# Kernel optimization log

Measured on AMD Instinct MI355X. Metric: run time of the kernel, lower is better.

Reference implementation:

```python
import jax, jax.numpy as jnp
import numpy as np

N = 50000      # nodes
F = 128        # in_features
OUT = 128      # out_features
E = 600000     # edges per adjacency (avg degree 12)
J = 2
BN_EPS = 1e-5


def setup_inputs() -> dict:
    key = jax.random.key(0)
    ks = jax.random.split(key, 10)
    x = jax.random.normal(ks[0], (N, F), dtype=jnp.float32)
    rows0 = jax.random.randint(ks[1], (E,), 0, N, dtype=jnp.int32)
    cols0 = jax.random.randint(ks[2], (E,), 0, N, dtype=jnp.int32)
    vals0 = jax.random.uniform(ks[3], (E,), dtype=jnp.float32)
    rows1 = jax.random.randint(ks[4], (E,), 0, N, dtype=jnp.int32)
    cols1 = jax.random.randint(ks[5], (E,), 0, N, dtype=jnp.int32)
    vals1 = jax.random.uniform(ks[6], (E,), dtype=jnp.float32)
    # Linear(J*F, OUT) params, torch default init U(-1/sqrt(fan_in), 1/sqrt(fan_in))
    lim = 1.0 / np.sqrt(J * F)
    W_fc = jax.random.uniform(ks[7], (OUT, J * F), dtype=jnp.float32, minval=-lim, maxval=lim)
    b_fc = jax.random.uniform(ks[8], (OUT,), dtype=jnp.float32, minval=-lim, maxval=lim)
    gamma = jnp.ones((OUT,), dtype=jnp.float32)
    beta = jnp.zeros((OUT,), dtype=jnp.float32)
    return {"x": x, "rows0": rows0, "cols0": cols0, "vals0": vals0,
            "rows1": rows1, "cols1": cols1, "vals1": vals1,
            "W_fc": W_fc, "b_fc": b_fc, "gamma": gamma, "beta": beta}


def _spmm(rows, cols, vals, x):
    # sparse [N,N] @ dense [N,F]: gather source features, weight, scatter-add to rows
    msgs = vals[:, None] * x[cols]                      # [E, F]
    return jax.ops.segment_sum(msgs, rows, num_segments=x.shape[0])  # [N, F]


def reference(x, rows0, cols0, vals0, rows1, cols1, vals1, W_fc, b_fc, gamma, beta):
    h = jnp.concatenate([_spmm(rows0, cols0, vals0, x),
                         _spmm(rows1, cols1, vals1, x)], axis=1)  # [N, J*F]
    y = h @ W_fc.T + b_fc                                         # [N, OUT]
    # BatchNorm1d (training mode: batch stats, biased variance)
    mean = jnp.mean(y, axis=0)
    var = jnp.mean((y - mean) ** 2, axis=0)
    return (y - mean) * jax.lax.rsqrt(var + BN_EPS) * gamma + beta
```

## Files before the change

### kernel.cpp

```cpp
#include <hip/hip_runtime.h>

#define N_NODES 50000
#define F_IN 128
#define OUT_F 128
#define JF 256
#define EDGES 600000
#define BN_EPS 1e-5f
#define MAXDEG 48
#define NPART 8
#define PART_ROWS 6250
#define CHUNK_E 2048
#define NCHUNK 586

#define SCAT_B (NPART * NCHUNK)
#define CONVX_B 6250
#define CONVW_B 32
#define BUILD_B (SCAT_B + CONVX_B + CONVW_B)
#define ROWS_PB 32
#define GATH_B 1563
#define GROWS 64
#define GEMM_B 782
#define HPAD 50048
#define NCOPY 16

typedef __attribute__((ext_vector_type(8))) short short8;
typedef __attribute__((ext_vector_type(4))) float floatx4;
typedef __attribute__((ext_vector_type(4))) unsigned short ushortx4;

static __device__ __forceinline__ unsigned short f2bf(float f) {
    unsigned int x = __float_as_uint(f);
    unsigned int r = (x + 0x7fffu + ((x >> 16) & 1u)) >> 16;
    return (unsigned short)r;
}
static __device__ __forceinline__ float bflo(unsigned int p) { return __uint_as_float(p << 16); }
static __device__ __forceinline__ float bfhi(unsigned int p) { return __uint_as_float(p & 0xffff0000u); }

__global__ __launch_bounds__(256) void build_kernel(
    const int* __restrict__ rows0, const int* __restrict__ cols0, const float* __restrict__ vals0,
    const int* __restrict__ rows1, const int* __restrict__ cols1, const float* __restrict__ vals1,
    int* __restrict__ cnt0, int* __restrict__ cnt1,
    unsigned int* __restrict__ pe0, unsigned int* __restrict__ pe1,
    const floatx4* __restrict__ x4, ushortx4* __restrict__ xb4,
    const float* __restrict__ W, uint2* __restrict__ Wb2)
{
    int bid = blockIdx.x;
    int tid = threadIdx.x;
    if (bid < SCAT_B) {
        unsigned part = (unsigned)(bid & (NPART - 1));
        int c0 = (bid >> 3) * CHUNK_E;

        bool pure0 = (c0 + CHUNK_E <= EDGES);
        bool pure1 = (c0 >= EDGES) && (c0 + CHUNK_E <= 2 * EDGES);
        if (pure0 || pure1) {
            const int*   rows = pure1 ? rows1 : rows0;
            const int*   cols = pure1 ? cols1 : cols0;
            const float* vals = pure1 ? vals1 : vals0;
            int*          cnt = pure1 ? cnt1 : cnt0;
            unsigned int*  pe = pure1 ? pe1 : pe0;
            int eb = pure1 ? c0 - EDGES : c0;
            #pragma unroll
            for (int g = 0; g < 2; ++g) {
                int e = eb + g * 1024 + tid * 4;
                int4 rv = *(const int4*)(rows + e);
                int rr[4] = {rv.x, rv.y, rv.z, rv.w};
                #pragma unroll
                for (int j = 0; j < 4; ++j) {
                    int r = rr[j];
                    if ((unsigned)r / (unsigned)PART_ROWS == part) {
                        int ee = e + j;
                        int c = cols[ee];
                        float v = vals[ee];
                        int p = atomicAdd(&cnt[r], 1);
                        if (p < MAXDEG)
                            pe[(size_t)r * MAXDEG + p] = ((unsigned int)c << 16) | f2bf(v);
                    }
                }
            }
        } else {
            for (int i = 0; i < CHUNK_E / 256; ++i) {
                int e = c0 + i * 256 + tid;
                if (e < 2 * EDGES) {
                    bool s1 = e >= EDGES;
                    int ee = s1 ? e - EDGES : e;
                    int r = s1 ? rows1[ee] : rows0[ee];
                    if ((unsigned)r / (unsigned)PART_ROWS == part) {
                        int c = s1 ? cols1[ee] : cols0[ee];
                        float v = s1 ? vals1[ee] : vals0[ee];
                        int* cnt = s1 ? cnt1 : cnt0;
                        unsigned int* pe = s1 ? pe1 : pe0;
                        int p = atomicAdd(&cnt[r], 1);
                        if (p < MAXDEG)
                            pe[(size_t)r * MAXDEG + p] = ((unsigned int)c << 16) | f2bf(v);
                    }
                }
            }
        }
    } else if (bid < SCAT_B + CONVX_B) {
        int i = (bid - SCAT_B) * 256 + tid;
        floatx4 v = __builtin_nontemporal_load(&x4[i]);
        ushortx4 o;
        o.x = f2bf(v.x); o.y = f2bf(v.y); o.z = f2bf(v.z); o.w = f2bf(v.w);
        __builtin_nontemporal_store(o, &xb4[i]);
    } else {
        int i = (bid - SCAT_B - CONVX_B) * 256 + tid;
        int col = i >> 6, l = i & 63;
        const float* wr = W + (size_t)col * JF;
        float a0 = wr[2 * l], a1 = wr[2 * l + 1];
        float b0 = wr[128 + 2 * l], b1 = wr[128 + 2 * l + 1];
        uint2 o;
        o.x = (unsigned int)f2bf(a0) | ((unsigned int)f2bf(a1) << 16);
        o.y = (unsigned int)f2bf(b0) | ((unsigned int)f2bf(b1) << 16);
        Wb2[col * 64 + l] = o;
    }
}

static __device__ __forceinline__ void rec_u(
    unsigned int q, int lane,
    const unsigned int* __restrict__ xb32, float& A0, float& A1)
{
    unsigned int xv = xb32[(q >> 16) * 64 + lane];
    float vv = __uint_as_float(q << 16);
    A0 += vv * bflo(xv);
    A1 += vv * bfhi(xv);
}
static __device__ __forceinline__ void rec_m(
    unsigned int q, bool on, int lane,
    const unsigned int* __restrict__ xb32, float& A0, float& A1)
{
    unsigned int idx = on ? (q >> 16) : 0u;
    float vv = on ? __uint_as_float(q << 16) : 0.0f;
    unsigned int xv = xb32[idx * 64 + lane];
    A0 += vv * bflo(xv);
    A1 += vv * bfhi(xv);
}

__global__ __launch_bounds__(256, 8) void gather_kernel(
    const unsigned int* __restrict__ xb32,
    const int* __restrict__ cnt0, const unsigned int* __restrict__ pe0,
    const int* __restrict__ cnt1, const unsigned int* __restrict__ pe1,
    uint2* __restrict__ hb)
{
    __shared__ uint4 recs[2][ROWS_PB][6];
    __shared__ int   lcnt[2][ROWS_PB];

    int tid = threadIdx.x;
    int lane = tid & 63;
    int w = tid >> 6;
    int wu = __builtin_amdgcn_readfirstlane(w);
    int row0 = blockIdx.x * ROWS_PB;

    {
        int idx = tid;
        #pragma unroll
        for (int pass = 0; pass < 2; ++pass) {
            if (idx < 384) {
                int lr = idx / 12;
                int rem = idx - lr * 12;
                int side = rem >= 6;
                int g = rem - side * 6;
                int r = row0 + lr; if (r >= N_NODES) r = N_NODES - 1;
                const unsigned int* pe = side ? pe1 : pe0;
                recs[side][lr][g] = *(const uint4*)(pe + (size_t)r * MAXDEG + g * 4);
            }
            idx += 256;
        }
        if (tid < 64) {
            int side = tid >= ROWS_PB;
            int lr = tid & (ROWS_PB - 1);
            int r = row0 + lr;
            int d = 0;
            if (r < N_NODES) d = (side ? cnt1 : cnt0)[r];
            if (d > MAXDEG) d = MAXDEG;
            lcnt[side][lr] = d;
        }
    }
    __syncthreads();

    for (int rr = 0; rr < 8; ++rr) {
        int lr = wu * 8 + rr;
        int r = row0 + lr;
        int d0 = __builtin_amdgcn_readfirstlane(lcnt[0][lr]);
        int d1 = __builtin_amdgcn_readfirstlane(lcnt[1][lr]);

        float aL0 = 0.f, aL1 = 0.f, aR0 = 0.f, aR1 = 0.f;

        #pragma unroll
        for (int g = 0; g < 6; ++g) {
            if (g * 4 < d0) {
                uint4 q = recs[0][lr][g];
                rec_u(q.x, lane, xb32, aL0, aL1);
                rec_m(q.y, g * 4 + 1 < d0, lane, xb32, aL0, aL1);
                rec_m(q.z, g * 4 + 2 < d0, lane, xb32, aL0, aL1);
                rec_m(q.w, g * 4 + 3 < d0, lane, xb32, aL0, aL1);
            }
        }
        #pragma unroll
        for (int g = 0; g < 6; ++g) {
            if (g * 4 < d1) {
                uint4 q = recs[1][lr][g];
                rec_u(q.x, lane, xb32, aR0, aR1);
                rec_m(q.y, g * 4 + 1 < d1, lane, xb32, aR0, aR1);
                rec_m(q.z, g * 4 + 2 < d1, lane, xb32, aR0, aR1);
                rec_m(q.w, g * 4 + 3 < d1, lane, xb32, aR0, aR1);
            }
        }
        if (d0 > 24)
            for (int p = 24; p < d0; ++p)
                rec_u(pe0[(size_t)r * MAXDEG + p], lane, xb32, aL0, aL1);
        if (d1 > 24)
            for (int p = 24; p < d1; ++p)
                rec_u(pe1[(size_t)r * MAXDEG + p], lane, xb32, aR0, aR1);

        uint2 o;
        o.x = (unsigned int)f2bf(aL0) | ((unsigned int)f2bf(aL1) << 16);
        o.y = (unsigned int)f2bf(aR0) | ((unsigned int)f2bf(aR1) << 16);
        hb[(size_t)(row0 + lr) * 64 + lane] = o;
    }
}

__global__ __launch_bounds__(256, 4) void gemm_kernel(
    const uint4* __restrict__ hb4,
    const ushort* __restrict__ Wb,
    const float* __restrict__ bias,
    float* __restrict__ y, float* __restrict__ stats)
{
    __shared__ char hsu[GROWS * 512];
    __shared__ float lstat[256];

    int tid = threadIdx.x;
    int lane = tid & 63;
    int w = tid >> 6;
    int row0 = blockIdx.x * GROWS;

    lstat[tid] = 0.f;

    const char* src = (const char*)hb4 + (size_t)row0 * 512;
    #pragma unroll
    for (int u = tid; u < GROWS * 32; u += 256) {
        int off = u * 16;
        int row = off >> 9;
        int dst = off ^ ((row & 7) << 4);
        *(uint4*)(hsu + dst) = *(const uint4*)(src + off);
    }
    __syncthreads();

    floatx4 acc[8];
    #pragma unroll
    for (int c = 0; c < 8; ++c) acc[c] = (floatx4){0.f, 0.f, 0.f, 0.f};

    int colb = lane & 15;
    int kg = lane >> 4;
    int arow = w * 16 + colb;
    unsigned int asw = (unsigned int)((arow & 7) << 4);

    #pragma unroll
    for (int k0 = 0; k0 < 8; ++k0) {
        short8 a = *(const short8*)(hsu + (((unsigned int)(arow * 512 + k0 * 64 + kg * 16)) ^ asw));
        #pragma unroll
        for (int c = 0; c < 8; ++c) {
            short8 b = *(const short8*)(Wb + (size_t)(c * 16 + colb) * 256 + k0 * 32 + kg * 8);
            acc[c] = __builtin_amdgcn_mfma_f32_16x16x32_bf16(a, b, acc[c], 0, 0, 0);
        }
    }

    int rq = kg * 4;
    #pragma unroll
    for (int c = 0; c < 8; ++c) {
        int col = c * 16 + colb;
        float bv = bias[col];
        float s = 0.f, s2 = 0.f;
        #pragma unroll
        for (int q = 0; q < 4; ++q) {
            int row = row0 + w * 16 + rq + q;
            if (row < N_NODES) {
                float val = acc[c][q] + bv;
                y[(size_t)row * OUT_F + col] = val;
                s += val; s2 += val * val;
            }
        }
        atomicAdd(&lstat[col], s);
        atomicAdd(&lstat[128 + col], s2);
    }
    __syncthreads();
    float* sdst = stats + (size_t)(blockIdx.x & (NCOPY - 1)) * 256;
    atomicAdd(&sdst[tid], lstat[tid]);
}

__global__ void bn_prep(const float* __restrict__ stats,
                        const float* __restrict__ gamma,
                        const float* __restrict__ beta,
                        float* __restrict__ ss)
{
    int o = threadIdx.x;
    if (o >= OUT_F) return;
    float s = 0.f, s2 = 0.f;
    #pragma unroll
    for (int c = 0; c < NCOPY; ++c) {
        s  += stats[c * 256 + o];
        s2 += stats[c * 256 + 128 + o];
    }
    float inv_n = 1.0f / (float)N_NODES;
    float mean = s * inv_n;
    float var  = s2 * inv_n - mean * mean;
    float sc = rsqrtf(var + BN_EPS) * gamma[o];
    ss[o] = sc;
    ss[OUT_F + o] = beta[o] - mean * sc;
}

__global__ __launch_bounds__(256) void bn_apply(
    float* __restrict__ y, const float* __restrict__ ss)
{
    size_t i = (size_t)blockIdx.x * blockDim.x + threadIdx.x;
    size_t total = (size_t)N_NODES * OUT_F / 4;
    if (i >= total) return;

    int c4 = (int)(i & (OUT_F / 4 - 1));
    float4 v  = ((const float4*)y)[i];
    float4 sc = ((const float4*)ss)[c4];
    float4 sh = ((const float4*)(ss + OUT_F))[c4];
    v.x = v.x * sc.x + sh.x;
    v.y = v.y * sc.y + sh.y;
    v.z = v.z * sc.z + sh.z;
    v.w = v.w * sc.w + sh.w;
    ((float4*)y)[i] = v;
}

extern "C" void kernel_launch(void* const* d_in, const int* in_sizes, int n_in,
                              void* d_out, int out_size, void* d_ws, size_t ws_size,
                              hipStream_t stream)
{
    const float* x     = (const float*)d_in[0];
    const int*   rows0 = (const int*)  d_in[1];
    const int*   cols0 = (const int*)  d_in[2];
    const float* vals0 = (const float*)d_in[3];
    const int*   rows1 = (const int*)  d_in[4];
    const int*   cols1 = (const int*)  d_in[5];
    const float* vals1 = (const float*)d_in[6];
    const float* W     = (const float*)d_in[7];
    const float* b     = (const float*)d_in[8];
    const float* gamma = (const float*)d_in[9];
    const float* beta  = (const float*)d_in[10];

    float* y = (float*)d_out;

    ushort* xb = (ushort*)d_ws;
    ushort* Wb = xb + (size_t)N_NODES * F_IN;
    unsigned int* pe0 = (unsigned int*)(Wb + OUT_F * JF);
    unsigned int* pe1 = pe0 + (size_t)N_NODES * MAXDEG;
    uint2* hb = (uint2*)(pe1 + (size_t)N_NODES * MAXDEG);
    int* cnt0 = (int*)(hb + (size_t)HPAD * 64);
    int* cnt1 = cnt0 + N_NODES;
    float* stats = (float*)(cnt1 + N_NODES);
    float* ss    = stats + NCOPY * 256;

    hipMemsetAsync(cnt0, 0, (2 * (size_t)N_NODES + NCOPY * 256) * sizeof(int), stream);

    build_kernel<<<BUILD_B, 256, 0, stream>>>(
        rows0, cols0, vals0, rows1, cols1, vals1,
        cnt0, cnt1, pe0, pe1,
        (const floatx4*)x, (ushortx4*)xb, W, (uint2*)Wb);

    gather_kernel<<<GATH_B, 256, 0, stream>>>(
        (const unsigned int*)xb, cnt0, pe0, cnt1, pe1, hb);

    gemm_kernel<<<GEMM_B, 256, 0, stream>>>(
        (const uint4*)hb, Wb, b, y, stats);

    bn_prep<<<1, 128, 0, stream>>>(stats, gamma, beta, ss);
    bn_apply<<<CONVX_B, 256, 0, stream>>>(y, ss);
}
```

Measured before the change: 182.1 us.

## Replace 8-pass partitioned edge scatter with two-phase bucket sort by row partition

```diff
diff --git a/kernel.cpp b/kernel.cpp
--- a/kernel.cpp
+++ b/kernel.cpp
@@ -9,15 +9,16 @@
 #define MAXDEG 48
 #define NPART 8
 #define PART_ROWS 6250
-#define CHUNK_E 2048
-#define NCHUNK 586
-
-#define SCAT_B (NPART * NCHUNK)
+#define BKCAP 163840
+#define LCAP 256
+#define EB_PER_SIDE 586
+#define EDGE_B (2*EB_PER_SIDE)
 #define CONVX_B 6250
 #define CONVW_B 32
-#define BUILD_B (SCAT_B + CONVX_B + CONVW_B)
-#define ROWS_PB 32
-#define GATH_B 1563
+#define BUILDA_B (EDGE_B + CONVX_B + CONVW_B)
+#define SCATB_B 1024
+#define ROWS_PB 16
+#define GATH_B 3125
 #define GROWS 64
 #define GEMM_B 782
 #define HPAD 50048
@@ -35,74 +36,75 @@
 static __device__ __forceinline__ float bflo(unsigned int p) { return __uint_as_float(p << 16); }
 static __device__ __forceinline__ float bfhi(unsigned int p) { return __uint_as_float(p & 0xffff0000u); }
 
-__global__ __launch_bounds__(256) void build_kernel(
+__global__ __launch_bounds__(256) void build_a(
     const int* __restrict__ rows0, const int* __restrict__ cols0, const float* __restrict__ vals0,
     const int* __restrict__ rows1, const int* __restrict__ cols1, const float* __restrict__ vals1,
-    int* __restrict__ cnt0, int* __restrict__ cnt1,
-    unsigned int* __restrict__ pe0, unsigned int* __restrict__ pe1,
+    uint2* __restrict__ buckets, int* __restrict__ gcur,
     const floatx4* __restrict__ x4, ushortx4* __restrict__ xb4,
     const float* __restrict__ W, uint2* __restrict__ Wb2)
 {
     int bid = blockIdx.x;
     int tid = threadIdx.x;
-    if (bid < SCAT_B) {
-        unsigned part = (unsigned)(bid & (NPART - 1));
-        int c0 = (bid >> 3) * CHUNK_E;
-
-        bool pure0 = (c0 + CHUNK_E <= EDGES);
-        bool pure1 = (c0 >= EDGES) && (c0 + CHUNK_E <= 2 * EDGES);
-        if (pure0 || pure1) {
-            const int*   rows = pure1 ? rows1 : rows0;
-            const int*   cols = pure1 ? cols1 : cols0;
-            const float* vals = pure1 ? vals1 : vals0;
-            int*          cnt = pure1 ? cnt1 : cnt0;
-            unsigned int*  pe = pure1 ? pe1 : pe0;
-            int eb = pure1 ? c0 - EDGES : c0;
+    if (bid < EDGE_B) {
+        __shared__ int   lcnt_[NPART];
+        __shared__ int   lbase[NPART];
+        __shared__ uint2 lbuf[NPART][LCAP];
+
+        if (tid < NPART) lcnt_[tid] = 0;
+        __syncthreads();
+
+        int side = bid >= EB_PER_SIDE;
+        int b = side ? bid - EB_PER_SIDE : bid;
+        const int*   rows = side ? rows1 : rows0;
+        const int*   cols = side ? cols1 : cols0;
+        const float* vals = side ? vals1 : vals0;
+
+        int e = b * 1024 + tid * 4;
+        if (e < EDGES) {
+            int4 rv = *(const int4*)(rows + e);
+            int4 cv = *(const int4*)(cols + e);
+            float4 vv = *(const float4*)(vals + e);
+            int rr[4] = {rv.x, rv.y, rv.z, rv.w};
+            int cc[4] = {cv.x, cv.y, cv.z, cv.w};
+            float ff[4] = {vv.x, vv.y, vv.z, vv.w};
             #pragma unroll
-            for (int g = 0; g < 2; ++g) {
-                int e = eb + g * 1024 + tid * 4;
-                int4 rv = *(const int4*)(rows + e);
-                int rr[4] = {rv.x, rv.y, rv.z, rv.w};
-                #pragma unroll
-                for (int j = 0; j < 4; ++j) {
-                    int r = rr[j];
-                    if ((unsigned)r / (unsigned)PART_ROWS == part) {
-                        int ee = e + j;
-                        int c = cols[ee];
-                        float v = vals[ee];
-                        int p = atomicAdd(&cnt[r], 1);
-                        if (p < MAXDEG)
-                            pe[(size_t)r * MAXDEG + p] = ((unsigned int)c << 16) | f2bf(v);
-                    }
+            for (int j = 0; j < 4; ++j) {
+                unsigned part = (unsigned)rr[j] / (unsigned)PART_ROWS;
+                uint2 q;
+                q.x = (unsigned)rr[j] | ((unsigned)side << 20);
+                q.y = ((unsigned)cc[j] << 16) | f2bf(ff[j]);
+                int pos = atomicAdd(&lcnt_[part], 1);
+                if (pos < LCAP) {
+                    lbuf[part][pos] = q;
+                } else {
+                    int gp = atomicAdd(&gcur[part], 1);
+                    if (gp < BKCAP) buckets[(size_t)part * BKCAP + gp] = q;
                 }
             }
-        } else {
-            for (int i = 0; i < CHUNK_E / 256; ++i) {
-                int e = c0 + i * 256 + tid;
-                if (e < 2 * EDGES) {
-                    bool s1 = e >= EDGES;
-                    int ee = s1 ? e - EDGES : e;
-                    int r = s1 ? rows1[ee] : rows0[ee];
-                    if ((unsigned)r / (unsigned)PART_ROWS == part) {
-                        int c = s1 ? cols1[ee] : cols0[ee];
-                        float v = s1 ? vals1[ee] : vals0[ee];
-                        int* cnt = s1 ? cnt1 : cnt0;
-                        unsigned int* pe = s1 ? pe1 : pe0;
-                        int p = atomicAdd(&cnt[r], 1);
-                        if (p < MAXDEG)
-                            pe[(size_t)r * MAXDEG + p] = ((unsigned int)c << 16) | f2bf(v);
-                    }
-                }
-            }
-        }
-    } else if (bid < SCAT_B + CONVX_B) {
-        int i = (bid - SCAT_B) * 256 + tid;
+        }
+        __syncthreads();
+        if (tid < NPART) {
+            int c = lcnt_[tid]; if (c > LCAP) c = LCAP;
+            lcnt_[tid] = c;
+            lbase[tid] = atomicAdd(&gcur[tid], c);
+        }
+        __syncthreads();
+        #pragma unroll
+        for (int p = 0; p < NPART; ++p) {
+            int c = lcnt_[p], base = lbase[p];
+            for (int j = tid; j < c; j += 256) {
+                int gp = base + j;
+                if (gp < BKCAP) buckets[(size_t)p * BKCAP + gp] = lbuf[p][j];
+            }
+        }
+    } else if (bid < EDGE_B + CONVX_B) {
+        int i = (bid - EDGE_B) * 256 + tid;
         floatx4 v = __builtin_nontemporal_load(&x4[i]);
         ushortx4 o;
         o.x = f2bf(v.x); o.y = f2bf(v.y); o.z = f2bf(v.z); o.w = f2bf(v.w);
         __builtin_nontemporal_store(o, &xb4[i]);
     } else {
-        int i = (bid - SCAT_B - CONVX_B) * 256 + tid;
+        int i = (bid - EDGE_B - CONVX_B) * 256 + tid;
         int col = i >> 6, l = i & 63;
         const float* wr = W + (size_t)col * JF;
         float a0 = wr[2 * l], a1 = wr[2 * l + 1];
@@ -114,6 +116,26 @@
     }
 }
 
+__global__ __launch_bounds__(256) void build_b(
+    const uint2* __restrict__ buckets, const int* __restrict__ gcur,
+    int* __restrict__ cnt0, int* __restrict__ cnt1,
+    unsigned int* __restrict__ pe0, unsigned int* __restrict__ pe1)
+{
+    int part = blockIdx.x & (NPART - 1);
+    int sub = blockIdx.x >> 3;
+    int n = gcur[part]; if (n > BKCAP) n = BKCAP;
+    const uint2* bk = buckets + (size_t)part * BKCAP;
+    for (int i = sub * 256 + threadIdx.x; i < n; i += (SCATB_B / NPART) * 256) {
+        uint2 q = bk[i];
+        unsigned r = q.x & 0xFFFFFu;
+        unsigned side = q.x >> 20;
+        int* cnt = side ? cnt1 : cnt0;
+        unsigned int* pe = side ? pe1 : pe0;
+        int p = atomicAdd(&cnt[r], 1);
+        if (p < MAXDEG) pe[(size_t)r * MAXDEG + p] = q.y;
+    }
+}
+
 static __device__ __forceinline__ void rec_u(
     unsigned int q, int lane,
     const unsigned int* __restrict__ xb32, float& A0, float& A1)
@@ -149,35 +171,25 @@
     int wu = __builtin_amdgcn_readfirstlane(w);
     int row0 = blockIdx.x * ROWS_PB;
 
-    {
-        int idx = tid;
-        #pragma unroll
-        for (int pass = 0; pass < 2; ++pass) {
-            if (idx < 384) {
-                int lr = idx / 12;
-                int rem = idx - lr * 12;
-                int side = rem >= 6;
-                int g = rem - side * 6;
-                int r = row0 + lr; if (r >= N_NODES) r = N_NODES - 1;
-                const unsigned int* pe = side ? pe1 : pe0;
-                recs[side][lr][g] = *(const uint4*)(pe + (size_t)r * MAXDEG + g * 4);
-            }
-            idx += 256;
-        }
-        if (tid < 64) {
-            int side = tid >= ROWS_PB;
-            int lr = tid & (ROWS_PB - 1);
-            int r = row0 + lr;
-            int d = 0;
-            if (r < N_NODES) d = (side ? cnt1 : cnt0)[r];
-            if (d > MAXDEG) d = MAXDEG;
-            lcnt[side][lr] = d;
-        }
+    if (tid < 192) {
+        int lr = tid / 12;
+        int rem = tid - lr * 12;
+        int side = rem >= 6;
+        int g = rem - side * 6;
+        const unsigned int* pe = side ? pe1 : pe0;
+        recs[side][lr][g] = *(const uint4*)(pe + (size_t)(row0 + lr) * MAXDEG + g * 4);
+    }
+    if (tid < 2 * ROWS_PB) {
+        int side = tid >= ROWS_PB;
+        int lr = tid & (ROWS_PB - 1);
+        int d = (side ? cnt1 : cnt0)[row0 + lr];
+        if (d > MAXDEG) d = MAXDEG;
+        lcnt[side][lr] = d;
     }
     __syncthreads();
 
-    for (int rr = 0; rr < 8; ++rr) {
-        int lr = wu * 8 + rr;
+    for (int rr = 0; rr < 4; ++rr) {
+        int lr = wu * 4 + rr;
         int r = row0 + lr;
         int d0 = __builtin_amdgcn_readfirstlane(lcnt[0][lr]);
         int d1 = __builtin_amdgcn_readfirstlane(lcnt[1][lr]);
@@ -214,7 +226,7 @@
         uint2 o;
         o.x = (unsigned int)f2bf(aL0) | ((unsigned int)f2bf(aL1) << 16);
         o.y = (unsigned int)f2bf(aR0) | ((unsigned int)f2bf(aR1) << 16);
-        hb[(size_t)(row0 + lr) * 64 + lane] = o;
+        hb[(size_t)r * 64 + lane] = o;
     }
 }
 
@@ -348,17 +360,23 @@
     unsigned int* pe0 = (unsigned int*)(Wb + OUT_F * JF);
     unsigned int* pe1 = pe0 + (size_t)N_NODES * MAXDEG;
     uint2* hb = (uint2*)(pe1 + (size_t)N_NODES * MAXDEG);
-    int* cnt0 = (int*)(hb + (size_t)HPAD * 64);
+    uint2* buckets = hb;
+    int* gcur = (int*)(hb + (size_t)HPAD * 64);
+    int* cnt0 = gcur + NPART;
     int* cnt1 = cnt0 + N_NODES;
     float* stats = (float*)(cnt1 + N_NODES);
     float* ss    = stats + NCOPY * 256;
 
-    hipMemsetAsync(cnt0, 0, (2 * (size_t)N_NODES + NCOPY * 256) * sizeof(int), stream);
-
-    build_kernel<<<BUILD_B, 256, 0, stream>>>(
+    hipMemsetAsync(gcur, 0,
+                   ((size_t)NPART + 2 * N_NODES + NCOPY * 256) * sizeof(int),
+                   stream);
+
+    build_a<<<BUILDA_B, 256, 0, stream>>>(
         rows0, cols0, vals0, rows1, cols1, vals1,
-        cnt0, cnt1, pe0, pe1,
+        buckets, gcur,
         (const floatx4*)x, (ushortx4*)xb, W, (uint2*)Wb);
+
+    build_b<<<SCATB_B, 256, 0, stream>>>(buckets, gcur, cnt0, cnt1, pe0, pe1);
 
     gather_kernel<<<GATH_B, 256, 0, stream>>>(
         (const unsigned int*)xb, cnt0, pe0, cnt1, pe1, hb);
```

New measurement: 193.0 us. 1.06x slower.

## Drop LDS staging in GEMM and split output columns across waves

Applied to the files above, without the earlier changes.

```diff
diff --git a/kernel.cpp b/kernel.cpp
--- a/kernel.cpp
+++ b/kernel.cpp
@@ -18,8 +18,8 @@
 #define BUILD_B (SCAT_B + CONVX_B + CONVW_B)
 #define ROWS_PB 32
 #define GATH_B 1563
-#define GROWS 64
-#define GEMM_B 782
+#define GEMM_ROWS 32
+#define GEMM_B 1563
 #define HPAD 50048
 #define NCOPY 16
 
@@ -204,10 +204,10 @@
                 rec_m(q.w, g * 4 + 3 < d1, lane, xb32, aR0, aR1);
             }
         }
-        if (d0 > 24)
+        if (d0 > 24 && r < N_NODES)
             for (int p = 24; p < d0; ++p)
                 rec_u(pe0[(size_t)r * MAXDEG + p], lane, xb32, aL0, aL1);
-        if (d1 > 24)
+        if (d1 > 24 && r < N_NODES)
             for (int p = 24; p < d1; ++p)
                 rec_u(pe1[(size_t)r * MAXDEG + p], lane, xb32, aR0, aR1);
 
@@ -218,60 +218,49 @@
     }
 }
 
-__global__ __launch_bounds__(256, 4) void gemm_kernel(
-    const uint4* __restrict__ hb4,
+__global__ __launch_bounds__(256, 6) void gemm_kernel(
+    const char* __restrict__ hb,
     const ushort* __restrict__ Wb,
     const float* __restrict__ bias,
     float* __restrict__ y, float* __restrict__ stats)
 {
-    __shared__ char hsu[GROWS * 512];
     __shared__ float lstat[256];
 
     int tid = threadIdx.x;
     int lane = tid & 63;
     int w = tid >> 6;
-    int row0 = blockIdx.x * GROWS;
+    int row0 = blockIdx.x * GEMM_ROWS + (w & 1) * 16;
+    int cbase = (w >> 1) * 64;
 
     lstat[tid] = 0.f;
-
-    const char* src = (const char*)hb4 + (size_t)row0 * 512;
-    #pragma unroll
-    for (int u = tid; u < GROWS * 32; u += 256) {
-        int off = u * 16;
-        int row = off >> 9;
-        int dst = off ^ ((row & 7) << 4);
-        *(uint4*)(hsu + dst) = *(const uint4*)(src + off);
-    }
     __syncthreads();
-
-    floatx4 acc[8];
-    #pragma unroll
-    for (int c = 0; c < 8; ++c) acc[c] = (floatx4){0.f, 0.f, 0.f, 0.f};
 
     int colb = lane & 15;
     int kg = lane >> 4;
-    int arow = w * 16 + colb;
-    unsigned int asw = (unsigned int)((arow & 7) << 4);
+    const char* abase = hb + (size_t)(row0 + colb) * 512 + kg * 16;
+
+    floatx4 acc[4];
+    #pragma unroll
+    for (int c = 0; c < 4; ++c) acc[c] = (floatx4){0.f, 0.f, 0.f, 0.f};
 
     #pragma unroll
     for (int k0 = 0; k0 < 8; ++k0) {
-        short8 a = *(const short8*)(hsu + (((unsigned int)(arow * 512 + k0 * 64 + kg * 16)) ^ asw));
-        #pragma unroll
-        for (int c = 0; c < 8; ++c) {
-            short8 b = *(const short8*)(Wb + (size_t)(c * 16 + colb) * 256 + k0 * 32 + kg * 8);
+        short8 a = *(const short8*)(abase + k0 * 64);
+        #pragma unroll
+        for (int c = 0; c < 4; ++c) {
+            short8 b = *(const short8*)(Wb + (size_t)(cbase + c * 16 + colb) * 256 + k0 * 32 + kg * 8);
             acc[c] = __builtin_amdgcn_mfma_f32_16x16x32_bf16(a, b, acc[c], 0, 0, 0);
         }
     }
 
-    int rq = kg * 4;
     #pragma unroll
-    for (int c = 0; c < 8; ++c) {
-        int col = c * 16 + colb;
+    for (int c = 0; c < 4; ++c) {
+        int col = cbase + c * 16 + colb;
         float bv = bias[col];
         float s = 0.f, s2 = 0.f;
         #pragma unroll
         for (int q = 0; q < 4; ++q) {
-            int row = row0 + w * 16 + rq + q;
+            int row = row0 + kg * 4 + q;
             if (row < N_NODES) {
                 float val = acc[c][q] + bv;
                 y[(size_t)row * OUT_F + col] = val;
@@ -353,7 +342,9 @@
     float* stats = (float*)(cnt1 + N_NODES);
     float* ss    = stats + NCOPY * 256;
 
-    hipMemsetAsync(cnt0, 0, (2 * (size_t)N_NODES + NCOPY * 256) * sizeof(int), stream);
+    hipMemsetAsync(cnt0, 0,
+                   (2 * (size_t)N_NODES + NCOPY * 256) * sizeof(int),
+                   stream);
 
     build_kernel<<<BUILD_B, 256, 0, stream>>>(
         rows0, cols0, vals0, rows1, cols1, vals1,
@@ -364,7 +355,7 @@
         (const unsigned int*)xb, cnt0, pe0, cnt1, pe1, hb);
 
     gemm_kernel<<<GEMM_B, 256, 0, stream>>>(
-        (const uint4*)hb, Wb, b, y, stats);
+        (const char*)hb, Wb, b, y, stats);
 
     bn_prep<<<1, 128, 0, stream>>>(stats, gamma, beta, ss);
     bn_apply<<<CONVX_B, 256, 0, stream>>>(y, ss);
```

After: 170.2 us. -6.5%, faster.
